# Optimization experiments

Measured on AMD Instinct MI355X. Metric: run time of the kernel, lower is better.

The kernel has to match this reference:

```python
import jax, jax.numpy as jnp
import numpy as np

N, E, G = 50000, 1600000, 64
IN, HID, OUT = 128, 64, 64
NEG_SLOPE = 0.2


def _p(key, shape):
    return jax.random.normal(key, shape, dtype=jnp.float32) * 0.1


def setup_inputs() -> dict:
    key = jax.random.key(0)
    ks = jax.random.split(key, 24)
    inp = {
        "x": jax.random.normal(ks[0], (N, IN), dtype=jnp.float32),
        "edge_index": jax.random.randint(ks[1], (2, E), 0, N),
        "edge_attr": jax.random.uniform(ks[2], (E, 1), dtype=jnp.float32),
        "batch": jnp.sort(jax.random.randint(ks[3], (N,), 0, G)),
        # GATv2 layer 1 (in=128 -> 64, heads=1)
        "Wl1": _p(ks[4], (IN, HID)), "bl1": _p(ks[5], (HID,)),
        "Wr1": _p(ks[6], (IN, HID)), "br1": _p(ks[7], (HID,)),
        "We1": _p(ks[8], (1, HID)), "att1": _p(ks[9], (HID,)), "bias1": _p(ks[10], (HID,)),
        # GATv2 layer 2 (64 -> 64)
        "Wl2": _p(ks[11], (HID, OUT)), "bl2": _p(ks[12], (OUT,)),
        "Wr2": _p(ks[13], (HID, OUT)), "br2": _p(ks[14], (OUT,)),
        "We2": _p(ks[15], (1, OUT)), "att2": _p(ks[16], (OUT,)), "bias2": _p(ks[17], (OUT,)),
        # MLP head: fc1 (64->32), bn1 (32), fc3 (32->1)
        "W_fc1": _p(ks[18], (OUT, OUT // 2)), "b_fc1": _p(ks[19], (OUT // 2,)),
        "bn_gamma": jnp.ones((OUT // 2,), jnp.float32),
        "bn_beta": jnp.zeros((OUT // 2,), jnp.float32),
        "bn_mean": _p(ks[20], (OUT // 2,)),
        "bn_var": jax.random.uniform(ks[21], (OUT // 2,), jnp.float32, 0.5, 1.5),
        "W_fc3": _p(ks[22], (OUT // 2, 1)), "b_fc3": _p(ks[23], (1,)),
    }
    return inp


def _add_self_loops(src, dst, edge_attr, n):
    # PyG add_self_loops with fill_value='mean': loop attr = mean of incoming edge attrs per node
    s = jax.ops.segment_sum(edge_attr, dst, num_segments=n)  # (N,1)
    c = jax.ops.segment_sum(jnp.ones((edge_attr.shape[0], 1), edge_attr.dtype), dst, num_segments=n)
    loop_attr = s / jnp.maximum(c, 1.0)
    loops = jnp.arange(n)
    return (jnp.concatenate([src, loops]), jnp.concatenate([dst, loops]),
            jnp.concatenate([edge_attr, loop_attr], axis=0))


def _gatv2(h, src, dst, e_attr, Wl, bl, Wr, br, We, att, bias, n):
    xl = h @ Wl + bl                     # (N, C) source transform
    xr = h @ Wr + br                     # (N, C) target transform
    ef = e_attr @ We                     # (E', C)
    s = jax.nn.leaky_relu(xl[src] + xr[dst] + ef, NEG_SLOPE)  # (E', C)
    logits = s @ att                     # (E',)
    m = jax.ops.segment_max(logits, dst, num_segments=n)
    m = jnp.where(jnp.isfinite(m), m, 0.0)
    p = jnp.exp(logits - m[dst])
    denom = jax.ops.segment_sum(p, dst, num_segments=n)
    alpha = p / (denom[dst] + 1e-16)
    out = jax.ops.segment_sum(alpha[:, None] * xl[src], dst, num_segments=n)
    return out + bias


def reference(x, edge_index, edge_attr, batch,
              Wl1, bl1, Wr1, br1, We1, att1, bias1,
              Wl2, bl2, Wr2, br2, We2, att2, bias2,
              W_fc1, b_fc1, bn_gamma, bn_beta, bn_mean, bn_var, W_fc3, b_fc3):
    n = x.shape[0]
    src, dst, ea = _add_self_loops(edge_index[0], edge_index[1], edge_attr, n)
    h = jax.nn.elu(_gatv2(x, src, dst, ea, Wl1, bl1, Wr1, br1, We1, att1, bias1, n))
    h = jax.nn.elu(_gatv2(h, src, dst, ea, Wl2, bl2, Wr2, br2, We2, att2, bias2, n))
    # global_mean_pool
    sums = jax.ops.segment_sum(h, batch, num_segments=G)
    cnts = jax.ops.segment_sum(jnp.ones((n, 1), h.dtype), batch, num_segments=G)
    pooled = sums / jnp.maximum(cnts, 1.0)
    # head: bn1(relu(fc1(.))) with eval-mode BN, dropout off, then fc3
    z = jax.nn.relu(pooled @ W_fc1 + b_fc1)
    z = (z - bn_mean) / jnp.sqrt(bn_var + 1e-5) * bn_gamma + bn_beta
    return z @ W_fc3 + b_fc3
```

## Files before the change

kernel.cpp:

```cpp
#include <hip/hip_runtime.h>
#include <hip/hip_fp16.h>
#include <math.h>

typedef unsigned long long u64;
typedef __attribute__((ext_vector_type(2))) _Float16 half2v;
typedef __attribute__((ext_vector_type(4))) _Float16 half4v;
typedef __attribute__((ext_vector_type(8))) _Float16 half8;
typedef __attribute__((ext_vector_type(4))) float f32x4;


#define CAP     12032
#define MAXSPAN 12288
#define PEPB    4096
#define NPWP    64

__global__ void k_prep_w(const float* __restrict__ Wl1, const float* __restrict__ bl1,
                         const float* __restrict__ Wr1, const float* __restrict__ br1,
                         const float* __restrict__ Wl2, const float* __restrict__ bl2,
                         const float* __restrict__ Wr2, const float* __restrict__ br2,
                         _Float16* __restrict__ Wt1, float* __restrict__ bv1,
                         _Float16* __restrict__ Wt2, float* __restrict__ bv2, int ld1) {
    int t = blockIdx.x * blockDim.x + threadIdx.x;
    int stride = gridDim.x * blockDim.x;
    int IN1 = 1 << ld1;
    for (int i = t; i < 128 * IN1; i += stride) {
        int n = i >> ld1, k = i & (IN1 - 1);
        float v = (n < 64) ? Wl1[k * 64 + n] : Wr1[k * 64 + (n - 64)];
        Wt1[n * IN1 + k] = (_Float16)v;
    }
    for (int i = t; i < 128 * 64; i += stride) {
        int n = i >> 6, k = i & 63;
        float v = (n < 64) ? Wl2[k * 64 + n] : Wr2[k * 64 + (n - 64)];
        Wt2[n * 64 + k] = (_Float16)v;
    }
    if (t < 128) {
        bv1[t] = (t < 64) ? bl1[t] : br1[t - 64];
        bv2[t] = (t < 64) ? bl2[t] : br2[t - 64];
    }
}

template<int IN>
__device__ __forceinline__ void xf_block_mfma(
        const float* __restrict__ h,
        const _Float16* __restrict__ Wt,
        const float* __restrict__ bv,
        __half* __restrict__ xl, __half* __restrict__ xr,
        int N, int node0, _Float16* rows, int t) {
    constexpr int LDK = IN + 8;
    constexpr int Q = IN / 4;
    for (int idx = t; idx < 64 * Q; idx += 256) {
        int nn = idx / Q;
        int kk = (idx % Q) * 4;
        int node = node0 + nn;
        float4 v = {0.f, 0.f, 0.f, 0.f};
        if (node < N) v = *(const float4*)(h + (size_t)node * IN + kk);
        half4v hv = {(_Float16)v.x, (_Float16)v.y, (_Float16)v.z, (_Float16)v.w};
        *(half4v*)(rows + nn * LDK + kk) = hv;
    }
    __syncthreads();
    int lane = t & 63, w = t >> 6;
    int n0w = w * 32;
    int lr = lane & 15, lq = lane >> 4;
    f32x4 acc[4][2];
#pragma unroll
    for (int i = 0; i < 4; ++i)
#pragma unroll
        for (int j = 0; j < 2; ++j) acc[i][j] = {0.f, 0.f, 0.f, 0.f};
    const _Float16* arow = rows + lr * LDK + lq * 8;
    const _Float16* brow = Wt + (size_t)(n0w + lr) * IN + lq * 8;
#pragma unroll
    for (int k0 = 0; k0 < IN; k0 += 32) {
        half8 a0 = *(const half8*)(arow + k0);
        half8 a1 = *(const half8*)(arow + 16 * LDK + k0);
        half8 a2 = *(const half8*)(arow + 32 * LDK + k0);
        half8 a3 = *(const half8*)(arow + 48 * LDK + k0);
        half8 b0 = *(const half8*)(brow + k0);
        half8 b1 = *(const half8*)(brow + 16 * IN + k0);
        acc[0][0] = __builtin_amdgcn_mfma_f32_16x16x32_f16(a0, b0, acc[0][0], 0, 0, 0);
        acc[1][0] = __builtin_amdgcn_mfma_f32_16x16x32_f16(a1, b0, acc[1][0], 0, 0, 0);
        acc[2][0] = __builtin_amdgcn_mfma_f32_16x16x32_f16(a2, b0, acc[2][0], 0, 0, 0);
        acc[3][0] = __builtin_amdgcn_mfma_f32_16x16x32_f16(a3, b0, acc[3][0], 0, 0, 0);
        acc[0][1] = __builtin_amdgcn_mfma_f32_16x16x32_f16(a0, b1, acc[0][1], 0, 0, 0);
        acc[1][1] = __builtin_amdgcn_mfma_f32_16x16x32_f16(a1, b1, acc[1][1], 0, 0, 0);
        acc[2][1] = __builtin_amdgcn_mfma_f32_16x16x32_f16(a2, b1, acc[2][1], 0, 0, 0);
        acc[3][1] = __builtin_amdgcn_mfma_f32_16x16x32_f16(a3, b1, acc[3][1], 0, 0, 0);
    }
    float bia0 = bv[n0w + lr];
    float bia1 = bv[n0w + 16 + lr];
#pragma unroll
    for (int ni = 0; ni < 2; ++ni) {
        int dim = n0w + ni * 16 + lr;
        __half* dst = (dim < 64) ? xl : xr;
        int dd = dim & 63;
        float bb = ni ? bia1 : bia0;
#pragma unroll
        for (int mi = 0; mi < 4; ++mi) {
#pragma unroll
            for (int r = 0; r < 4; ++r) {
                int node = node0 + mi * 16 + lq * 4 + r;
                if (node < N)
                    dst[((size_t)node << 6) + dd] = __float2half(acc[mi][ni][r] + bb);
            }
        }
    }
}

union XfPartSmem {
    _Float16 rows[64 * 136];
    struct { int lh[256]; int lbase[256]; int lcur[256]; } p;
};

template<int IN>
__global__ void k_xf1_part(
        const float* __restrict__ h,
        const _Float16* __restrict__ Wt, const float* __restrict__ bv,
        __half* __restrict__ xl, __half* __restrict__ xr, int N, int nbXF,
        const int* __restrict__ ei, const float* __restrict__ ea,
        int* __restrict__ qtail, u64* __restrict__ queue, int E) {
    __shared__ XfPartSmem sm;
    int t = threadIdx.x;
    if (blockIdx.x < nbXF) {
        xf_block_mfma<IN>(h, Wt, bv, xl, xr, N, blockIdx.x * 64, sm.rows, t);
    } else {
        int pb = blockIdx.x - nbXF;
        sm.p.lh[t] = 0; sm.p.lcur[t] = 0;
        __syncthreads();
        int base = pb * PEPB;
        int end = base + PEPB; if (end > E) end = E;
        for (int e = base + t; e < end; e += 256) {
            int d = ei[E + e];
            atomicAdd(&sm.p.lh[d >> 8], 1);
        }
        __syncthreads();
        if (sm.p.lh[t]) sm.p.lbase[t] = atomicAdd(&qtail[t], sm.p.lh[t]);
        __syncthreads();
        for (int e = base + t; e < end; e += 256) {
            int d = ei[E + e];
            int src = ei[e];
            float a = ea[e];
            int b = d >> 8;
            int idx = atomicAdd(&sm.p.lcur[b], 1);
            unsigned aq = (unsigned)(a * 16777216.0f);
            queue[(size_t)b * CAP + sm.p.lbase[b] + idx] =
                (((u64)aq) << 25) | (((u64)(d & 255)) << 17) | (unsigned)src;
        }
    }
}

__device__ __forceinline__ unsigned attr_q15(float a) {
    unsigned short hb = __builtin_bit_cast(unsigned short, (_Float16)a);
    return (unsigned)(hb >> 1);
}

__global__ void __launch_bounds__(1024)
k_build(const u64* __restrict__ queue, const int* __restrict__ qtail,
        u64* __restrict__ rs2, unsigned* __restrict__ csr, int N) {
    __shared__ u64 stat[256];
    __shared__ int fill[256], sc[256];
    __shared__ unsigned lcsr[MAXSPAN];
    int t = threadIdx.x, b = blockIdx.x;
    if (t < 256) stat[t] = 0;
    __syncthreads();
    int cnt = qtail[b];
    size_t q0 = (size_t)b * CAP;
    for (int i = t; i < cnt; i += 1024) {
        u64 r = queue[q0 + i];
        int dl = (int)((r >> 17) & 255);
        atomicAdd(&stat[dl], (1ULL << 32) | (unsigned)(r >> 25));
    }
    __syncthreads();
    int dg = (b << 8) + t;
    u64 p = (t < 256) ? stat[t] : 0;
    int deg = (int)(p >> 32);
    int v = (t < 256 && dg < N) ? deg + 1 : 0;
    if (t < 256) sc[t] = v;
    __syncthreads();
    for (int off = 1; off < 256; off <<= 1) {
        int a = (t >= off && t < 256) ? sc[t - off] : 0;
        __syncthreads();
        if (t < 256) sc[t] += a;
        __syncthreads();
    }
    int c0 = b * MAXSPAN;
    if (t < 256 && dg < N) {
        int basel = sc[t] - v;
        rs2[dg] = (u64)(unsigned)(c0 + basel) | (((u64)(unsigned)(c0 + basel + deg + 1)) << 32);
        fill[t] = basel;
        float mean = ((float)(unsigned)p * (1.0f / 16777216.0f)) / fmaxf((float)deg, 1.0f);
        if (basel + deg < MAXSPAN) lcsr[basel + deg] = (attr_q15(mean) << 17) | (unsigned)dg;
    }
    __syncthreads();
    for (int i = t; i < cnt; i += 1024) {
        u64 r = queue[q0 + i];
        int dl = (int)((r >> 17) & 255);
        int pos = atomicAdd(&fill[dl], 1);
        float av = (float)(unsigned)(r >> 25) * (1.0f / 16777216.0f);
        if (pos < MAXSPAN) lcsr[pos] = (attr_q15(av) << 17) | (unsigned)(r & 0x1FFFFu);
    }
    __syncthreads();
    int span = sc[255];
    if (span > MAXSPAN) span = MAXSPAN;
    for (int j = t; j < span; j += 1024) csr[c0 + j] = lcsr[j];
}

__global__ void k_node_xf(const float* __restrict__ h,
                          const _Float16* __restrict__ Wt, const float* __restrict__ bv,
                          __half* __restrict__ xl, __half* __restrict__ xr, int N) {
    __shared__ _Float16 rows[64 * 72];
    xf_block_mfma<64>(h, Wt, bv, xl, xr, N, blockIdx.x * 64, rows, threadIdx.x);
}

template<int CTRL>
__device__ __forceinline__ float dpp_add(float c) {
    int t = __builtin_amdgcn_update_dpp(0, __builtin_bit_cast(int, c),
                                        CTRL, 0xF, 0xF, true);
    return c + __builtin_bit_cast(float, t);
}

#define EDGE_GROUP(r, xh, cc)                                                  \
    {                                                                          \
        _Float16 ah = __builtin_bit_cast(_Float16, (unsigned short)((r >> 16) & 0xFFFEu)); \
        half2v aa = {ah, ah};                                                  \
        half2v x01 = {xh.x, xh.y}, x23 = {xh.z, xh.w};                         \
        half2v v01 = aa * We01 + (x01 + xr01);                                 \
        half2v v23 = aa * We23 + (x23 + xr23);                                 \
        half2v s01 = __builtin_elementwise_max(v01, v01 * k02);                \
        half2v s23 = __builtin_elementwise_max(v23, v23 * k02);                \
        cc = __builtin_amdgcn_fdot2(s01, at01, 0.f, false);                    \
        cc = __builtin_amdgcn_fdot2(s23, at23, cc, false);                     \
    }

__global__ void k_attn(const __half* __restrict__ xl, const __half* __restrict__ xr,
                       const unsigned* __restrict__ csr, const u64* __restrict__ rs2,
                       const float* __restrict__ We, const float* __restrict__ att,
                       const float* __restrict__ bias,
                       float* __restrict__ hout, int N) {
    int lane = threadIdx.x & 63;
    int d = (int)(((size_t)blockIdx.x * blockDim.x + threadIdx.x) >> 6);
    if (d >= N) return;
    int eq = lane >> 4;
    int fl = lane & 15;
    float4 Wef  = *(const float4*)(We + fl * 4);
    float4 attf = *(const float4*)(att + fl * 4);
    half2v We01 = {(_Float16)Wef.x, (_Float16)Wef.y};
    half2v We23 = {(_Float16)Wef.z, (_Float16)Wef.w};
    half2v at01 = {(_Float16)attf.x, (_Float16)attf.y};
    half2v at23 = {(_Float16)attf.z, (_Float16)attf.w};
    half4v xrh = *(const half4v*)(xr + ((size_t)d << 6) + fl * 4);
    half2v xr01 = {xrh.x, xrh.y}, xr23 = {xrh.z, xrh.w};
    const half2v k02 = {(_Float16)0.2f, (_Float16)0.2f};
    u64 rr = rs2[d];
    int e0 = __builtin_amdgcn_readfirstlane((int)(unsigned)rr);
    int e1 = __builtin_amdgcn_readfirstlane((int)(unsigned)(rr >> 32));
    float l = 0.f;
    float4 O = {0.f, 0.f, 0.f, 0.f};
    int e = e0;
    for (; e + 16 <= e1; e += 16) {
        unsigned rA = csr[e + eq];
        unsigned rB = csr[e + 4 + eq];
        unsigned rC = csr[e + 8 + eq];
        unsigned rD = csr[e + 12 + eq];
        half4v xA = *(const half4v*)(xl + (((size_t)(rA & 0x1FFFFu)) << 6) + fl * 4);
        half4v xB = *(const half4v*)(xl + (((size_t)(rB & 0x1FFFFu)) << 6) + fl * 4);
        half4v xC = *(const half4v*)(xl + (((size_t)(rC & 0x1FFFFu)) << 6) + fl * 4);
        half4v xD = *(const half4v*)(xl + (((size_t)(rD & 0x1FFFFu)) << 6) + fl * 4);
        float cA, cB, cC, cD;
        EDGE_GROUP(rA, xA, cA);
        EDGE_GROUP(rB, xB, cB);
        EDGE_GROUP(rC, xC, cC);
        EDGE_GROUP(rD, xD, cD);
        cA = dpp_add<0xB1>(cA);  cB = dpp_add<0xB1>(cB);
        cC = dpp_add<0xB1>(cC);  cD = dpp_add<0xB1>(cD);
        cA = dpp_add<0x4E>(cA);  cB = dpp_add<0x4E>(cB);
        cC = dpp_add<0x4E>(cC);  cD = dpp_add<0x4E>(cD);
        cA = dpp_add<0x141>(cA); cB = dpp_add<0x141>(cB);
        cC = dpp_add<0x141>(cC); cD = dpp_add<0x141>(cD);
        cA = dpp_add<0x140>(cA); cB = dpp_add<0x140>(cB);
        cC = dpp_add<0x140>(cC); cD = dpp_add<0x140>(cD);
        float qA = __expf(cA), qB = __expf(cB), qC = __expf(cC), qD = __expf(cD);
        l += (qA + qB) + (qC + qD);
        O.x = fmaf(qA, (float)xA.x, O.x); O.x = fmaf(qB, (float)xB.x, O.x);
        O.x = fmaf(qC, (float)xC.x, O.x); O.x = fmaf(qD, (float)xD.x, O.x);
        O.y = fmaf(qA, (float)xA.y, O.y); O.y = fmaf(qB, (float)xB.y, O.y);
        O.y = fmaf(qC, (float)xC.y, O.y); O.y = fmaf(qD, (float)xD.y, O.y);
        O.z = fmaf(qA, (float)xA.z, O.z); O.z = fmaf(qB, (float)xB.z, O.z);
        O.z = fmaf(qC, (float)xC.z, O.z); O.z = fmaf(qD, (float)xD.z, O.z);
        O.w = fmaf(qA, (float)xA.w, O.w); O.w = fmaf(qB, (float)xB.w, O.w);
        O.w = fmaf(qC, (float)xC.w, O.w); O.w = fmaf(qD, (float)xD.w, O.w);
    }
    for (; e < e1; e += 4) {
        int ee = e + eq;
        bool valid = ee < e1;
        unsigned r = csr[valid ? ee : (e1 - 1)];
        half4v xh = *(const half4v*)(xl + (((size_t)(r & 0x1FFFFu)) << 6) + fl * 4);
        float c;
        EDGE_GROUP(r, xh, c);
        c = dpp_add<0xB1>(c);
        c = dpp_add<0x4E>(c);
        c = dpp_add<0x141>(c);
        c = dpp_add<0x140>(c);
        float q = valid ? __expf(c) : 0.f;
        l += q;
        O.x = fmaf(q, (float)xh.x, O.x);
        O.y = fmaf(q, (float)xh.y, O.y);
        O.z = fmaf(q, (float)xh.z, O.z);
        O.w = fmaf(q, (float)xh.w, O.w);
    }
#pragma unroll
    for (int mm = 16; mm <= 32; mm <<= 1) {
        l   += __shfl_xor(l, mm, 64);
        O.x += __shfl_xor(O.x, mm, 64);
        O.y += __shfl_xor(O.y, mm, 64);
        O.z += __shfl_xor(O.z, mm, 64);
        O.w += __shfl_xor(O.w, mm, 64);
    }
    if (eq == 0) {
        float inv = 1.0f / (l + 1e-16f);
        float4 b4 = *(const float4*)(bias + fl * 4);
        float4 res;
        res.x = fmaf(O.x, inv, b4.x);
        res.y = fmaf(O.y, inv, b4.y);
        res.z = fmaf(O.z, inv, b4.z);
        res.w = fmaf(O.w, inv, b4.w);
        res.x = res.x > 0.f ? res.x : expm1f(res.x);
        res.y = res.y > 0.f ? res.y : expm1f(res.y);
        res.z = res.z > 0.f ? res.z : expm1f(res.z);
        res.w = res.w > 0.f ? res.w : expm1f(res.w);
        *(float4*)(hout + ((size_t)d << 6) + fl * 4) = res;
    }
}

__global__ void k_pool_head(const float* __restrict__ h, const int* __restrict__ batch,
                            float* __restrict__ pooled, float* __restrict__ gcnt,
                            int N, int* __restrict__ done,
                            const float* __restrict__ W1, const float* __restrict__ b1,
                            const float* __restrict__ gam, const float* __restrict__ bet,
                            const float* __restrict__ mu, const float* __restrict__ var,
                            const float* __restrict__ W3, const float* __restrict__ b3,
                            float* __restrict__ out, int G) {
    int tid = threadIdx.x;
    int lane = tid & 63;
    int wave = (int)(((size_t)blockIdx.x * blockDim.x + tid) >> 6);
    int begin = wave * NPWP;
    if (begin < N) {
        int bidx = begin + lane;
        int bval = batch[bidx < N ? bidx : (N - 1)];
        float hv[NPWP];
#pragma unroll
        for (int j = 0; j < NPWP; ++j) {
            int n = begin + j;
            hv[j] = (n < N) ? h[((size_t)n << 6) + lane] : 0.f;
        }
        int g = __shfl(bval, 0, 64);
        float acc = 0.f, cnt = 0.f;
#pragma unroll
        for (int j = 0; j < NPWP; ++j) {
            if (begin + j < N) {
                int gn = __shfl(bval, j, 64);
                if (gn != g) {
                    atomicAdd(&pooled[((size_t)g << 6) + lane], acc);
                    if (lane == 0) atomicAdd(&gcnt[g], cnt);
                    g = gn; acc = 0.f; cnt = 0.f;
                }
                acc += hv[j];
                cnt += 1.f;
            }
        }
        atomicAdd(&pooled[((size_t)g << 6) + lane], acc);
        if (lane == 0) atomicAdd(&gcnt[g], cnt);
    }
    __threadfence();
    __syncthreads();
    __shared__ int lastFlag;
    if (tid == 0) lastFlag = (atomicAdd(done, 1) == (int)gridDim.x - 1);
    __syncthreads();
    if (lastFlag && tid < G) {
        __threadfence();
        int g = tid;
        float inv = 1.0f / fmaxf(gcnt[g], 1.0f);
        float pr[64];
        for (int k = 0; k < 64; ++k) pr[k] = pooled[((size_t)g << 6) + k] * inv;
        float o = b3[0];
        for (int j = 0; j < 32; ++j) {
            float z = b1[j];
            for (int k = 0; k < 64; ++k) z += pr[k] * W1[k * 32 + j];
            z = fmaxf(z, 0.f);
            z = (z - mu[j]) / sqrtf(var[j] + 1e-5f) * gam[j] + bet[j];
            o += z * W3[j];
        }
        out[g] = o;
    }
}

extern "C" void kernel_launch(void* const* d_in, const int* in_sizes, int n_in,
                              void* d_out, int out_size, void* d_ws, size_t ws_size,
                              hipStream_t stream) {
    const float* x    = (const float*)d_in[0];
    const int*   ei   = (const int*)d_in[1];
    const float* ea   = (const float*)d_in[2];
    const int*   batch= (const int*)d_in[3];
    const float* Wl1  = (const float*)d_in[4];
    const float* bl1  = (const float*)d_in[5];
    const float* Wr1  = (const float*)d_in[6];
    const float* br1  = (const float*)d_in[7];
    const float* We1  = (const float*)d_in[8];
    const float* att1 = (const float*)d_in[9];
    const float* bi1  = (const float*)d_in[10];
    const float* Wl2  = (const float*)d_in[11];
    const float* bl2  = (const float*)d_in[12];
    const float* Wr2  = (const float*)d_in[13];
    const float* br2  = (const float*)d_in[14];
    const float* We2  = (const float*)d_in[15];
    const float* att2 = (const float*)d_in[16];
    const float* bi2  = (const float*)d_in[17];
    const float* Wf1  = (const float*)d_in[18];
    const float* bf1  = (const float*)d_in[19];
    const float* gam  = (const float*)d_in[20];
    const float* bet  = (const float*)d_in[21];
    const float* mu   = (const float*)d_in[22];
    const float* var  = (const float*)d_in[23];
    const float* Wf3  = (const float*)d_in[24];
    const float* bf3  = (const float*)d_in[25];

    const int N    = in_sizes[3];
    const int E    = in_sizes[2];
    const int INd  = in_sizes[0] / N;
    const int ld1  = (INd == 128) ? 7 : 6;
    const int G    = out_size;
    const int NB   = (N + 255) / 256;

    char* w = (char*)d_ws;
    auto carve = [&](size_t bytes) { char* p = w; w += (bytes + 255) & ~(size_t)255; return p; };
    __half*   xl       = (__half*)  carve((size_t)N * 64 * 2);
    __half*   xr       = (__half*)  carve((size_t)N * 64 * 2);
    float*    hbuf     = (float*)   carve((size_t)N * 64 * 4);
    unsigned* csr      = (unsigned*)carve((size_t)NB * MAXSPAN * 4);
    u64*      queue    = (u64*)     carve((size_t)NB * CAP * 8);
    u64*      rs2      = (u64*)     carve((size_t)N * 8);
    int*      qtail    = (int*)     carve((size_t)(NB + 1) * 4);
    float*    pooled   = (float*)   carve((size_t)G * 64 * 4);
    float*    gcnt     = (float*)   carve((size_t)G * 4);
    int*      done     = (int*)     carve(256);
    _Float16* Wt1      = (_Float16*)carve((size_t)128 * 128 * 2);
    float*    bv1      = (float*)   carve(128 * 4);
    _Float16* Wt2      = (_Float16*)carve((size_t)128 * 64 * 2);
    float*    bv2      = (float*)   carve(128 * 4);

    const int TB = 256;
    const int nbXF = (N + 63) / 64;
    const int attnBlocks = (N + 3) / 4;
    const int nbPart = (E + PEPB - 1) / PEPB;

    hipMemsetAsync(qtail, 0, (size_t)(NB + 1) * 4, stream);
    size_t poolRegion = (((size_t)G * 64 * 4 + 255) & ~(size_t)255)
                      + (((size_t)G * 4 + 255) & ~(size_t)255) + 256;
    hipMemsetAsync(pooled, 0, poolRegion, stream);

    k_prep_w<<<32, TB, 0, stream>>>(Wl1, bl1, Wr1, br1, Wl2, bl2, Wr2, br2,
                                    Wt1, bv1, Wt2, bv2, ld1);

    if (INd == 128)
        k_xf1_part<128><<<nbXF + nbPart, TB, 0, stream>>>(x, Wt1, bv1, xl, xr, N, nbXF,
                                                          ei, ea, qtail, queue, E);
    else
        k_xf1_part<64><<<nbXF + nbPart, TB, 0, stream>>>(x, Wt1, bv1, xl, xr, N, nbXF,
                                                         ei, ea, qtail, queue, E);
    k_build<<<NB, 1024, 0, stream>>>(queue, qtail, rs2, csr, N);

    k_attn<<<attnBlocks, TB, 0, stream>>>(xl, xr, csr, rs2, We1, att1, bi1, hbuf, N);

    k_node_xf<<<nbXF, TB, 0, stream>>>(hbuf, Wt2, bv2, xl, xr, N);
    k_attn<<<attnBlocks, TB, 0, stream>>>(xl, xr, csr, rs2, We2, att2, bi2, hbuf, N);

    const int poolWaves = (N + NPWP - 1) / NPWP;
    k_pool_head<<<(poolWaves * 64 + TB - 1) / TB, TB, 0, stream>>>(
        hbuf, batch, pooled, gcnt, N, done,
        Wf1, bf1, gam, bet, mu, var, Wf3, bf3, (float*)d_out, G);
}
```

Before: 304.5 us.

## Use 64-node CSR buckets with 4-aligned segments and vectorised attention loads

```diff
diff --git a/kernel.cpp b/kernel.cpp
--- a/kernel.cpp
+++ b/kernel.cpp
@@ -7,10 +7,12 @@
 typedef __attribute__((ext_vector_type(4))) _Float16 half4v;
 typedef __attribute__((ext_vector_type(8))) _Float16 half8;
 typedef __attribute__((ext_vector_type(4))) float f32x4;
-
-
-#define CAP     12032
-#define MAXSPAN 12288
+typedef __attribute__((ext_vector_type(2))) float f32x2;
+
+
+#define BKT     64
+#define CAP     3008
+#define MAXSPAN 3392
 #define PEPB    4096
 #define NPWP    64
 
@@ -107,7 +109,7 @@
 
 union XfPartSmem {
     _Float16 rows[64 * 136];
-    struct { int lh[256]; int lbase[256]; int lcur[256]; } p;
+    struct { int lh[1024]; int lbase[1024]; int lcur[1024]; } p;
 };
 
 template<int IN>
@@ -123,26 +125,27 @@
         xf_block_mfma<IN>(h, Wt, bv, xl, xr, N, blockIdx.x * 64, sm.rows, t);
     } else {
         int pb = blockIdx.x - nbXF;
-        sm.p.lh[t] = 0; sm.p.lcur[t] = 0;
+        for (int i = t; i < 1024; i += 256) { sm.p.lh[i] = 0; sm.p.lcur[i] = 0; }
         __syncthreads();
         int base = pb * PEPB;
         int end = base + PEPB; if (end > E) end = E;
         for (int e = base + t; e < end; e += 256) {
             int d = ei[E + e];
-            atomicAdd(&sm.p.lh[d >> 8], 1);
+            atomicAdd(&sm.p.lh[d >> 6], 1);
         }
         __syncthreads();
-        if (sm.p.lh[t]) sm.p.lbase[t] = atomicAdd(&qtail[t], sm.p.lh[t]);
+        for (int i = t; i < 1024; i += 256)
+            if (sm.p.lh[i]) sm.p.lbase[i] = atomicAdd(&qtail[i], sm.p.lh[i]);
         __syncthreads();
         for (int e = base + t; e < end; e += 256) {
             int d = ei[E + e];
             int src = ei[e];
             float a = ea[e];
-            int b = d >> 8;
+            int b = d >> 6;
             int idx = atomicAdd(&sm.p.lcur[b], 1);
             unsigned aq = (unsigned)(a * 16777216.0f);
             queue[(size_t)b * CAP + sm.p.lbase[b] + idx] =
-                (((u64)aq) << 25) | (((u64)(d & 255)) << 17) | (unsigned)src;
+                (((u64)aq) << 25) | (((u64)(d & 63)) << 17) | (unsigned)src;
         }
     }
 }
@@ -155,34 +158,34 @@
 __global__ void __launch_bounds__(1024)
 k_build(const u64* __restrict__ queue, const int* __restrict__ qtail,
         u64* __restrict__ rs2, unsigned* __restrict__ csr, int N) {
-    __shared__ u64 stat[256];
-    __shared__ int fill[256], sc[256];
+    __shared__ u64 stat[BKT];
+    __shared__ int fill[BKT], sc[BKT];
     __shared__ unsigned lcsr[MAXSPAN];
     int t = threadIdx.x, b = blockIdx.x;
-    if (t < 256) stat[t] = 0;
+    if (t < BKT) stat[t] = 0;
     __syncthreads();
     int cnt = qtail[b];
     size_t q0 = (size_t)b * CAP;
     for (int i = t; i < cnt; i += 1024) {
         u64 r = queue[q0 + i];
-        int dl = (int)((r >> 17) & 255);
+        int dl = (int)((r >> 17) & (BKT - 1));
         atomicAdd(&stat[dl], (1ULL << 32) | (unsigned)(r >> 25));
     }
     __syncthreads();
-    int dg = (b << 8) + t;
-    u64 p = (t < 256) ? stat[t] : 0;
+    int dg = b * BKT + t;
+    u64 p = (t < BKT) ? stat[t] : 0;
     int deg = (int)(p >> 32);
-    int v = (t < 256 && dg < N) ? deg + 1 : 0;
-    if (t < 256) sc[t] = v;
-    __syncthreads();
-    for (int off = 1; off < 256; off <<= 1) {
-        int a = (t >= off && t < 256) ? sc[t - off] : 0;
+    int v = (t < BKT && dg < N) ? ((deg + 1 + 3) & ~3) : 0;
+    if (t < BKT) sc[t] = v;
+    __syncthreads();
+    for (int off = 1; off < BKT; off <<= 1) {
+        int a = (t >= off && t < BKT) ? sc[t - off] : 0;
         __syncthreads();
-        if (t < 256) sc[t] += a;
+        if (t < BKT) sc[t] += a;
         __syncthreads();
     }
     int c0 = b * MAXSPAN;
-    if (t < 256 && dg < N) {
+    if (t < BKT && dg < N) {
         int basel = sc[t] - v;
         rs2[dg] = (u64)(unsigned)(c0 + basel) | (((u64)(unsigned)(c0 + basel + deg + 1)) << 32);
         fill[t] = basel;
@@ -192,13 +195,13 @@
     __syncthreads();
     for (int i = t; i < cnt; i += 1024) {
         u64 r = queue[q0 + i];
-        int dl = (int)((r >> 17) & 255);
+        int dl = (int)((r >> 17) & (BKT - 1));
         int pos = atomicAdd(&fill[dl], 1);
         float av = (float)(unsigned)(r >> 25) * (1.0f / 16777216.0f);
         if (pos < MAXSPAN) lcsr[pos] = (attr_q15(av) << 17) | (unsigned)(r & 0x1FFFFu);
     }
     __syncthreads();
-    int span = sc[255];
+    int span = sc[BKT - 1];
     if (span > MAXSPAN) span = MAXSPAN;
     for (int j = t; j < span; j += 1024) csr[c0 + j] = lcsr[j];
 }
@@ -240,35 +243,38 @@
     if (d >= N) return;
     int eq = lane >> 4;
     int fl = lane & 15;
+    const float LOG2E = 1.44269504088896340736f;
     float4 Wef  = *(const float4*)(We + fl * 4);
     float4 attf = *(const float4*)(att + fl * 4);
     half2v We01 = {(_Float16)Wef.x, (_Float16)Wef.y};
     half2v We23 = {(_Float16)Wef.z, (_Float16)Wef.w};
-    half2v at01 = {(_Float16)attf.x, (_Float16)attf.y};
-    half2v at23 = {(_Float16)attf.z, (_Float16)attf.w};
-    half4v xrh = *(const half4v*)(xr + ((size_t)d << 6) + fl * 4);
+    half2v at01 = {(_Float16)(attf.x * LOG2E), (_Float16)(attf.y * LOG2E)};
+    half2v at23 = {(_Float16)(attf.z * LOG2E), (_Float16)(attf.w * LOG2E)};
+    unsigned flo = (unsigned)fl * 4u;
+    half4v xrh = *(const half4v*)(xr + (((unsigned)d << 6) | flo));
     half2v xr01 = {xrh.x, xrh.y}, xr23 = {xrh.z, xrh.w};
     const half2v k02 = {(_Float16)0.2f, (_Float16)0.2f};
     u64 rr = rs2[d];
     int e0 = __builtin_amdgcn_readfirstlane((int)(unsigned)rr);
     int e1 = __builtin_amdgcn_readfirstlane((int)(unsigned)(rr >> 32));
     float l = 0.f;
-    float4 O = {0.f, 0.f, 0.f, 0.f};
+    f32x2 Oa = {0.f, 0.f}, Ob = {0.f, 0.f};
     int e = e0;
     for (; e + 16 <= e1; e += 16) {
-        unsigned rA = csr[e + eq];
-        unsigned rB = csr[e + 4 + eq];
-        unsigned rC = csr[e + 8 + eq];
-        unsigned rD = csr[e + 12 + eq];
-        half4v xA = *(const half4v*)(xl + (((size_t)(rA & 0x1FFFFu)) << 6) + fl * 4);
-        half4v xB = *(const half4v*)(xl + (((size_t)(rB & 0x1FFFFu)) << 6) + fl * 4);
-        half4v xC = *(const half4v*)(xl + (((size_t)(rC & 0x1FFFFu)) << 6) + fl * 4);
-        half4v xD = *(const half4v*)(xl + (((size_t)(rD & 0x1FFFFu)) << 6) + fl * 4);
+        uint4 rv = *(const uint4*)(csr + e + (eq << 2));
+        unsigned oA = ((rv.x & 0x1FFFFu) << 6) | flo;
+        unsigned oB = ((rv.y & 0x1FFFFu) << 6) | flo;
+        unsigned oC = ((rv.z & 0x1FFFFu) << 6) | flo;
+        unsigned oD = ((rv.w & 0x1FFFFu) << 6) | flo;
+        half4v xA = *(const half4v*)(xl + oA);
+        half4v xB = *(const half4v*)(xl + oB);
+        half4v xC = *(const half4v*)(xl + oC);
+        half4v xD = *(const half4v*)(xl + oD);
         float cA, cB, cC, cD;
-        EDGE_GROUP(rA, xA, cA);
-        EDGE_GROUP(rB, xB, cB);
-        EDGE_GROUP(rC, xC, cC);
-        EDGE_GROUP(rD, xD, cD);
+        EDGE_GROUP(rv.x, xA, cA);
+        EDGE_GROUP(rv.y, xB, cB);
+        EDGE_GROUP(rv.z, xC, cC);
+        EDGE_GROUP(rv.w, xD, cD);
         cA = dpp_add<0xB1>(cA);  cB = dpp_add<0xB1>(cB);
         cC = dpp_add<0xB1>(cC);  cD = dpp_add<0xB1>(cD);
         cA = dpp_add<0x4E>(cA);  cB = dpp_add<0x4E>(cB);
@@ -277,55 +283,61 @@
         cC = dpp_add<0x141>(cC); cD = dpp_add<0x141>(cD);
         cA = dpp_add<0x140>(cA); cB = dpp_add<0x140>(cB);
         cC = dpp_add<0x140>(cC); cD = dpp_add<0x140>(cD);
-        float qA = __expf(cA), qB = __expf(cB), qC = __expf(cC), qD = __expf(cD);
+        float qA = __builtin_exp2f(cA), qB = __builtin_exp2f(cB);
+        float qC = __builtin_exp2f(cC), qD = __builtin_exp2f(cD);
         l += (qA + qB) + (qC + qD);
-        O.x = fmaf(qA, (float)xA.x, O.x); O.x = fmaf(qB, (float)xB.x, O.x);
-        O.x = fmaf(qC, (float)xC.x, O.x); O.x = fmaf(qD, (float)xD.x, O.x);
-        O.y = fmaf(qA, (float)xA.y, O.y); O.y = fmaf(qB, (float)xB.y, O.y);
-        O.y = fmaf(qC, (float)xC.y, O.y); O.y = fmaf(qD, (float)xD.y, O.y);
-        O.z = fmaf(qA, (float)xA.z, O.z); O.z = fmaf(qB, (float)xB.z, O.z);
-        O.z = fmaf(qC, (float)xC.z, O.z); O.z = fmaf(qD, (float)xD.z, O.z);
-        O.w = fmaf(qA, (float)xA.w, O.w); O.w = fmaf(qB, (float)xB.w, O.w);
-        O.w = fmaf(qC, (float)xC.w, O.w); O.w = fmaf(qD, (float)xD.w, O.w);
+        f32x2 qA2 = {qA, qA}, qB2 = {qB, qB}, qC2 = {qC, qC}, qD2 = {qD, qD};
+        f32x2 xa01 = {(float)xA.x, (float)xA.y}, xa23 = {(float)xA.z, (float)xA.w};
+        f32x2 xb01 = {(float)xB.x, (float)xB.y}, xb23 = {(float)xB.z, (float)xB.w};
+        f32x2 xc01 = {(float)xC.x, (float)xC.y}, xc23 = {(float)xC.z, (float)xC.w};
+        f32x2 xd01 = {(float)xD.x, (float)xD.y}, xd23 = {(float)xD.z, (float)xD.w};
+        Oa = __builtin_elementwise_fma(qA2, xa01, Oa);
+        Oa = __builtin_elementwise_fma(qB2, xb01, Oa);
+        Oa = __builtin_elementwise_fma(qC2, xc01, Oa);
+        Oa = __builtin_elementwise_fma(qD2, xd01, Oa);
+        Ob = __builtin_elementwise_fma(qA2, xa23, Ob);
+        Ob = __builtin_elementwise_fma(qB2, xb23, Ob);
+        Ob = __builtin_elementwise_fma(qC2, xc23, Ob);
+        Ob = __builtin_elementwise_fma(qD2, xd23, Ob);
     }
     for (; e < e1; e += 4) {
         int ee = e + eq;
         bool valid = ee < e1;
         unsigned r = csr[valid ? ee : (e1 - 1)];
-        half4v xh = *(const half4v*)(xl + (((size_t)(r & 0x1FFFFu)) << 6) + fl * 4);
+        half4v xh = *(const half4v*)(xl + (((r & 0x1FFFFu) << 6) | flo));
         float c;
         EDGE_GROUP(r, xh, c);
         c = dpp_add<0xB1>(c);
         c = dpp_add<0x4E>(c);
         c = dpp_add<0x141>(c);
         c = dpp_add<0x140>(c);
-        float q = valid ? __expf(c) : 0.f;
+        float q = valid ? __builtin_exp2f(c) : 0.f;
         l += q;
-        O.x = fmaf(q, (float)xh.x, O.x);
-        O.y = fmaf(q, (float)xh.y, O.y);
-        O.z = fmaf(q, (float)xh.z, O.z);
-        O.w = fmaf(q, (float)xh.w, O.w);
+        Oa.x = fmaf(q, (float)xh.x, Oa.x);
+        Oa.y = fmaf(q, (float)xh.y, Oa.y);
+        Ob.x = fmaf(q, (float)xh.z, Ob.x);
+        Ob.y = fmaf(q, (float)xh.w, Ob.y);
     }
 #pragma unroll
     for (int mm = 16; mm <= 32; mm <<= 1) {
-        l   += __shfl_xor(l, mm, 64);
-        O.x += __shfl_xor(O.x, mm, 64);
-        O.y += __shfl_xor(O.y, mm, 64);
-        O.z += __shfl_xor(O.z, mm, 64);
-        O.w += __shfl_xor(O.w, mm, 64);
+        l    += __shfl_xor(l, mm, 64);
+        Oa.x += __shfl_xor(Oa.x, mm, 64);
+        Oa.y += __shfl_xor(Oa.y, mm, 64);
+        Ob.x += __shfl_xor(Ob.x, mm, 64);
+        Ob.y += __shfl_xor(Ob.y, mm, 64);
     }
     if (eq == 0) {
         float inv = 1.0f / (l + 1e-16f);
         float4 b4 = *(const float4*)(bias + fl * 4);
         float4 res;
-        res.x = fmaf(O.x, inv, b4.x);
-        res.y = fmaf(O.y, inv, b4.y);
-        res.z = fmaf(O.z, inv, b4.z);
-        res.w = fmaf(O.w, inv, b4.w);
-        res.x = res.x > 0.f ? res.x : expm1f(res.x);
-        res.y = res.y > 0.f ? res.y : expm1f(res.y);
-        res.z = res.z > 0.f ? res.z : expm1f(res.z);
-        res.w = res.w > 0.f ? res.w : expm1f(res.w);
+        res.x = fmaf(Oa.x, inv, b4.x);
+        res.y = fmaf(Oa.y, inv, b4.y);
+        res.z = fmaf(Ob.x, inv, b4.z);
+        res.w = fmaf(Ob.y, inv, b4.w);
+        res.x = res.x > 0.f ? res.x : __expf(res.x) - 1.f;
+        res.y = res.y > 0.f ? res.y : __expf(res.y) - 1.f;
+        res.z = res.z > 0.f ? res.z : __expf(res.z) - 1.f;
+        res.w = res.w > 0.f ? res.w : __expf(res.w) - 1.f;
         *(float4*)(hout + ((size_t)d << 6) + fl * 4) = res;
     }
 }
@@ -427,7 +439,7 @@
     const int INd  = in_sizes[0] / N;
     const int ld1  = (INd == 128) ? 7 : 6;
     const int G    = out_size;
-    const int NB   = (N + 255) / 256;
+    const int NB   = (N + BKT - 1) / BKT;
 
     char* w = (char*)d_ws;
     auto carve = [&](size_t bytes) { char* p = w; w += (bytes + 255) & ~(size_t)255; return p; };
```

Measured after the change: 313.7 us. 1.03x slower.
